# Kernel tuning notes

Hardware: AMD Instinct MI355X
Metric: run time of the kernel (lower is better)

The kernel has to match this reference:

```python
import jax, jax.numpy as jnp
import numpy as np

CEN_IN, DIR_IN, CEN_K, DIR_K = 32, 32, 3, 5
B, H, W = 32, 128, 128
C = CEN_IN + 4 * DIR_IN  # central + 4 directional channel groups


def build_kernel(cen_tensor, dir_tensor):
    """Assemble the dense [C, K, K] depthwise kernel (K = dir_k).

    Central channels: cen_k x cen_k patch centered in a K x K zero kernel.
    Directional channels: 1D taps of length K placed along the middle row
    (horizontal), middle column (vertical), main diagonal, anti-diagonal.
    """
    K = DIR_K
    pad = (K - CEN_K) // 2
    mid = K // 2
    cen = jnp.zeros((CEN_IN, K, K), cen_tensor.dtype)
    cen = cen.at[:, pad:pad + CEN_K, pad:pad + CEN_K].set(cen_tensor)
    z = jnp.zeros((DIR_IN, K, K), dir_tensor.dtype)
    horiz = z.at[:, mid, :].set(dir_tensor)
    vert = z.at[:, :, mid].set(dir_tensor)
    diag = jax.vmap(jnp.diag)(dir_tensor)          # taps on main diagonal
    adiag = jnp.flip(diag, axis=-1)                # taps on anti-diagonal
    return jnp.concatenate([cen, horiz, vert, diag, adiag], axis=0)  # [C, K, K]


def setup_inputs() -> dict:
    key = jax.random.key(0)
    kx, kc, kd = jax.random.split(key, 3)
    x = jax.random.normal(kx, (B, C, H, W), dtype=jnp.float32)
    cen_tensor = jax.random.normal(kc, (CEN_IN, CEN_K, CEN_K), dtype=jnp.float32)
    dir_tensor = jax.random.normal(kd, (DIR_IN, DIR_K), dtype=jnp.float32)
    return {"x": x, "cen_tensor": cen_tensor, "dir_tensor": dir_tensor}


def reference(x, cen_tensor, dir_tensor):
    w = build_kernel(cen_tensor, dir_tensor)[:, None, :, :]  # [C, 1, K, K]
    return jax.lax.conv_general_dilated(
        x, w,
        window_strides=(1, 1),
        padding="SAME",
        feature_group_count=C,
        dimension_numbers=("NCHW", "OIHW", "NCHW"),
    )
```

## Files before the change

kernel.cpp:

```cpp
#include <hip/hip_runtime.h>


#define Hc 128
#define Wc 128
#define Cc 160

__device__ __forceinline__ float ldx(const float* __restrict__ row, int w) {
    return ((unsigned)w < (unsigned)Wc) ? row[w] : 0.0f;
}

__global__ __launch_bounds__(256) void ddw_kernel(
    const float* __restrict__ x, const float* __restrict__ cen,
    const float* __restrict__ dir, float* __restrict__ out)
{
    const int plane = blockIdx.y;
    const int c = plane % Cc;
    const float* __restrict__ xp = x + (size_t)plane * (Hc * Wc);
    float* __restrict__ op = out + (size_t)plane * (Hc * Wc);

    const int tid = threadIdx.x;
    const int r  = blockIdx.x * 8 + (tid >> 5);
    const int w0 = (tid & 31) << 2;

    float a0 = 0.f, a1 = 0.f, a2 = 0.f, a3 = 0.f;
    const int grp = c >> 5;

    if (grp == 0) {
        const float* cw = cen + c * 9;
        float k[9];
        #pragma unroll
        for (int i = 0; i < 9; i++) k[i] = cw[i];
        #pragma unroll
        for (int dh = -1; dh <= 1; dh++) {
            int hh = r + dh;
            if ((unsigned)hh >= (unsigned)Hc) continue;
            const float* row = xp + hh * Wc;
            float4 m = *(const float4*)(row + w0);
            float v0 = ldx(row, w0 - 1);
            float v5 = ldx(row, w0 + 4);
            const float* kk = k + (dh + 1) * 3;
            a0 += kk[0] * v0  + kk[1] * m.x + kk[2] * m.y;
            a1 += kk[0] * m.x + kk[1] * m.y + kk[2] * m.z;
            a2 += kk[0] * m.y + kk[1] * m.z + kk[2] * m.w;
            a3 += kk[0] * m.z + kk[1] * m.w + kk[2] * v5;
        }
    } else {
        const float* dw = dir + (c & 31) * 5;
        float d[5];
        #pragma unroll
        for (int i = 0; i < 5; i++) d[i] = dw[i];

        if (grp == 1) {
            const float* row = xp + r * Wc;
            float4 m = *(const float4*)(row + w0);
            float v[8];
            v[0] = ldx(row, w0 - 2); v[1] = ldx(row, w0 - 1);
            v[2] = m.x; v[3] = m.y; v[4] = m.z; v[5] = m.w;
            v[6] = ldx(row, w0 + 4); v[7] = ldx(row, w0 + 5);
            #pragma unroll
            for (int t = 0; t < 5; t++) {
                a0 += d[t] * v[t];
                a1 += d[t] * v[t + 1];
                a2 += d[t] * v[t + 2];
                a3 += d[t] * v[t + 3];
            }
        } else if (grp == 2) {
            #pragma unroll
            for (int t = 0; t < 5; t++) {
                int hh = r + t - 2;
                if ((unsigned)hh >= (unsigned)Hc) continue;
                float4 m = *(const float4*)(xp + hh * Wc + w0);
                a0 += d[t] * m.x; a1 += d[t] * m.y;
                a2 += d[t] * m.z; a3 += d[t] * m.w;
            }
        } else if (grp == 3) {
            #pragma unroll
            for (int t = 0; t < 5; t++) {
                int hh = r + t - 2;
                if ((unsigned)hh >= (unsigned)Hc) continue;
                const float* row = xp + hh * Wc;
                int wb = w0 + t - 2;
                a0 += d[t] * ldx(row, wb);
                a1 += d[t] * ldx(row, wb + 1);
                a2 += d[t] * ldx(row, wb + 2);
                a3 += d[t] * ldx(row, wb + 3);
            }
        } else {
            #pragma unroll
            for (int t = 0; t < 5; t++) {
                int hh = r + t - 2;
                if ((unsigned)hh >= (unsigned)Hc) continue;
                const float* row = xp + hh * Wc;
                int wb = w0 + 2 - t;
                a0 += d[t] * ldx(row, wb);
                a1 += d[t] * ldx(row, wb + 1);
                a2 += d[t] * ldx(row, wb + 2);
                a3 += d[t] * ldx(row, wb + 3);
            }
        }
    }

    float4 res = make_float4(a0, a1, a2, a3);
    *(float4*)(op + r * Wc + w0) = res;
}

extern "C" void kernel_launch(void* const* d_in, const int* in_sizes, int n_in,
                              void* d_out, int out_size, void* d_ws, size_t ws_size,
                              hipStream_t stream) {
    const float* x   = (const float*)d_in[0];
    const float* cen = (const float*)d_in[1];
    const float* dir = (const float*)d_in[2];
    float* out = (float*)d_out;

    dim3 grid(Hc / 8, 32 * Cc);
    ddw_kernel<<<grid, 256, 0, stream>>>(x, cen, dir, out);
}
```

Baseline: 577.7 us.

## Stage input row tile with halo in shared memory for depthwise conv

Each block now loads its 8 output rows plus a 2-row halo into an LDS tile padded with zero columns, then computes every channel-group stencil from shared memory. This replaces repeated, bounds-checked global loads with one coalesced float4 load per element and branch-free LDS reads. In exchange it adds a block-wide barrier and LDS traffic, and it loads 12 rows even for groups that need fewer. The kernel is memory-bound, and the earlier global reloads were probably already served from cache.

Measured after the change: 527.3 us. 8.7% less time.

```diff
diff --git a/kernel.cpp b/kernel.cpp
--- a/kernel.cpp
+++ b/kernel.cpp
@@ -4,45 +4,60 @@
 #define Hc 128
 #define Wc 128
 #define Cc 160
-
-__device__ __forceinline__ float ldx(const float* __restrict__ row, int w) {
-    return ((unsigned)w < (unsigned)Wc) ? row[w] : 0.0f;
-}
+#define TR 8
+#define LW 136
 
 __global__ __launch_bounds__(256) void ddw_kernel(
     const float* __restrict__ x, const float* __restrict__ cen,
     const float* __restrict__ dir, float* __restrict__ out)
 {
+    __shared__ float t[(TR + 4) * LW];
+
     const int plane = blockIdx.y;
     const int c = plane % Cc;
     const float* __restrict__ xp = x + (size_t)plane * (Hc * Wc);
     float* __restrict__ op = out + (size_t)plane * (Hc * Wc);
 
     const int tid = threadIdx.x;
-    const int r  = blockIdx.x * 8 + (tid >> 5);
+    const int r0 = blockIdx.x * TR;
+
+    if (tid < 48) {
+        int row = tid >> 2, j = tid & 3;
+        int l = (j < 2) ? (2 + j) : (130 + j);
+        t[row * LW + l] = 0.0f;
+    }
+    #pragma unroll
+    for (int it = 0; it < 2; ++it) {
+        int s = tid + it * 256;
+        if (s < 12 * 32) {
+            int row = s >> 5, q = s & 31;
+            int gr = r0 - 2 + row;
+            float4 v = make_float4(0.f, 0.f, 0.f, 0.f);
+            if ((unsigned)gr < (unsigned)Hc)
+                v = *(const float4*)(xp + gr * Wc + (q << 2));
+            *(float4*)&t[row * LW + 4 + (q << 2)] = v;
+        }
+    }
+    __syncthreads();
+
+    const int rl = tid >> 5;
     const int w0 = (tid & 31) << 2;
+    const float* __restrict__ trow = &t[(rl + 2) * LW + (w0 + 4)];
 
     float a0 = 0.f, a1 = 0.f, a2 = 0.f, a3 = 0.f;
     const int grp = c >> 5;
 
     if (grp == 0) {
         const float* cw = cen + c * 9;
-        float k[9];
         #pragma unroll
-        for (int i = 0; i < 9; i++) k[i] = cw[i];
-        #pragma unroll
-        for (int dh = -1; dh <= 1; dh++) {
-            int hh = r + dh;
-            if ((unsigned)hh >= (unsigned)Hc) continue;
-            const float* row = xp + hh * Wc;
-            float4 m = *(const float4*)(row + w0);
-            float v0 = ldx(row, w0 - 1);
-            float v5 = ldx(row, w0 + 4);
-            const float* kk = k + (dh + 1) * 3;
-            a0 += kk[0] * v0  + kk[1] * m.x + kk[2] * m.y;
-            a1 += kk[0] * m.x + kk[1] * m.y + kk[2] * m.z;
-            a2 += kk[0] * m.y + kk[1] * m.z + kk[2] * m.w;
-            a3 += kk[0] * m.z + kk[1] * m.w + kk[2] * v5;
+        for (int dh = 0; dh < 3; dh++) {
+            const float* rr = trow + (dh - 1) * LW;
+            float v0 = rr[-1], v1 = rr[0], v2 = rr[1], v3 = rr[2], v4 = rr[3], v5 = rr[4];
+            float k0 = cw[dh * 3 + 0], k1 = cw[dh * 3 + 1], k2 = cw[dh * 3 + 2];
+            a0 += k0 * v0 + k1 * v1 + k2 * v2;
+            a1 += k0 * v1 + k1 * v2 + k2 * v3;
+            a2 += k0 * v2 + k1 * v3 + k2 * v4;
+            a3 += k0 * v3 + k1 * v4 + k2 * v5;
         }
     } else {
         const float* dw = dir + (c & 31) * 5;
@@ -51,57 +66,45 @@
         for (int i = 0; i < 5; i++) d[i] = dw[i];
 
         if (grp == 1) {
-            const float* row = xp + r * Wc;
-            float4 m = *(const float4*)(row + w0);
             float v[8];
-            v[0] = ldx(row, w0 - 2); v[1] = ldx(row, w0 - 1);
-            v[2] = m.x; v[3] = m.y; v[4] = m.z; v[5] = m.w;
-            v[6] = ldx(row, w0 + 4); v[7] = ldx(row, w0 + 5);
             #pragma unroll
-            for (int t = 0; t < 5; t++) {
-                a0 += d[t] * v[t];
-                a1 += d[t] * v[t + 1];
-                a2 += d[t] * v[t + 2];
-                a3 += d[t] * v[t + 3];
+            for (int i = 0; i < 8; i++) v[i] = trow[i - 2];
+            #pragma unroll
+            for (int tt = 0; tt < 5; tt++) {
+                a0 += d[tt] * v[tt];
+                a1 += d[tt] * v[tt + 1];
+                a2 += d[tt] * v[tt + 2];
+                a3 += d[tt] * v[tt + 3];
             }
         } else if (grp == 2) {
             #pragma unroll
-            for (int t = 0; t < 5; t++) {
-                int hh = r + t - 2;
-                if ((unsigned)hh >= (unsigned)Hc) continue;
-                float4 m = *(const float4*)(xp + hh * Wc + w0);
-                a0 += d[t] * m.x; a1 += d[t] * m.y;
-                a2 += d[t] * m.z; a3 += d[t] * m.w;
+            for (int tt = 0; tt < 5; tt++) {
+                float4 m = *(const float4*)(trow + (tt - 2) * LW);
+                a0 += d[tt] * m.x; a1 += d[tt] * m.y;
+                a2 += d[tt] * m.z; a3 += d[tt] * m.w;
             }
         } else if (grp == 3) {
             #pragma unroll
-            for (int t = 0; t < 5; t++) {
-                int hh = r + t - 2;
-                if ((unsigned)hh >= (unsigned)Hc) continue;
-                const float* row = xp + hh * Wc;
-                int wb = w0 + t - 2;
-                a0 += d[t] * ldx(row, wb);
-                a1 += d[t] * ldx(row, wb + 1);
-                a2 += d[t] * ldx(row, wb + 2);
-                a3 += d[t] * ldx(row, wb + 3);
+            for (int tt = 0; tt < 5; tt++) {
+                const float* rr = trow + (tt - 2) * LW + (tt - 2);
+                a0 += d[tt] * rr[0];
+                a1 += d[tt] * rr[1];
+                a2 += d[tt] * rr[2];
+                a3 += d[tt] * rr[3];
             }
         } else {
             #pragma unroll
-            for (int t = 0; t < 5; t++) {
-                int hh = r + t - 2;
-                if ((unsigned)hh >= (unsigned)Hc) continue;
-                const float* row = xp + hh * Wc;
-                int wb = w0 + 2 - t;
-                a0 += d[t] * ldx(row, wb);
-                a1 += d[t] * ldx(row, wb + 1);
-                a2 += d[t] * ldx(row, wb + 2);
-                a3 += d[t] * ldx(row, wb + 3);
+            for (int tt = 0; tt < 5; tt++) {
+                const float* rr = trow + (tt - 2) * LW + (2 - tt);
+                a0 += d[tt] * rr[0];
+                a1 += d[tt] * rr[1];
+                a2 += d[tt] * rr[2];
+                a3 += d[tt] * rr[3];
             }
         }
     }
 
-    float4 res = make_float4(a0, a1, a2, a3);
-    *(float4*)(op + r * Wc + w0) = res;
+    *(float4*)(op + (r0 + rl) * Wc + w0) = make_float4(a0, a1, a2, a3);
 }
 
 extern "C" void kernel_launch(void* const* d_in, const int* in_sizes, int n_in,
@@ -112,6 +115,6 @@
     const float* dir = (const float*)d_in[2];
     float* out = (float*)d_out;
 
-    dim3 grid(Hc / 8, 32 * Cc);
+    dim3 grid(Hc / TR, 32 * Cc);
     ddw_kernel<<<grid, 256, 0, stream>>>(x, cen, dir, out);
 }
```
